# Optimization experiments

Measured on AMD Instinct MI355X. Metric: run time of the kernel, lower is better.

Reference implementation:

```python
import jax, jax.numpy as jnp
import numpy as np

H = 128  # hidden_size
I = 28   # input_size
C = 10   # num_classes


def setup_inputs() -> dict:
    key = jax.random.key(0)
    ks = jax.random.split(key, 11)
    s = 1.0 / np.sqrt(H)  # torch nn.RNN init scale
    return {
        "x": jax.random.normal(ks[0], (8192, 28, I), dtype=jnp.float32),
        "W_ih0": jax.random.uniform(ks[1], (H, I), jnp.float32, -s, s),
        "W_hh0": jax.random.uniform(ks[2], (H, H), jnp.float32, -s, s),
        "b_ih0": jax.random.uniform(ks[3], (H,), jnp.float32, -s, s),
        "b_hh0": jax.random.uniform(ks[4], (H,), jnp.float32, -s, s),
        "W_ih1": jax.random.uniform(ks[5], (H, H), jnp.float32, -s, s),
        "W_hh1": jax.random.uniform(ks[6], (H, H), jnp.float32, -s, s),
        "b_ih1": jax.random.uniform(ks[7], (H,), jnp.float32, -s, s),
        "b_hh1": jax.random.uniform(ks[8], (H,), jnp.float32, -s, s),
        "fc_w": jax.random.uniform(ks[9], (C, H), jnp.float32, -s, s),
        "fc_b": jax.random.uniform(ks[10], (C,), jnp.float32, -s, s),
    }


def _rnn_layer_full(x, W_ih, b_ih, W_hh, b_hh):
    # x: [B, T, D] -> full output sequence [B, T, H]
    B = x.shape[0]
    h0 = jnp.zeros((B, H), x.dtype)
    xw = jnp.einsum('btd,hd->bth', x, W_ih) + b_ih  # precompute input GEMM

    def step(h, xw_t):
        h = jnp.tanh(xw_t + h @ W_hh.T + b_hh)
        return h, h

    _, ys = jax.lax.scan(step, h0, jnp.swapaxes(xw, 0, 1))  # [T, B, H]
    return jnp.swapaxes(ys, 0, 1)


def _rnn_layer_last(x, W_ih, b_ih, W_hh, b_hh):
    # only the final hidden state is needed downstream
    B = x.shape[0]
    h0 = jnp.zeros((B, H), x.dtype)
    xw = jnp.einsum('btd,hd->bth', x, W_ih) + b_ih

    def step(h, xw_t):
        h = jnp.tanh(xw_t + h @ W_hh.T + b_hh)
        return h, None

    h_last, _ = jax.lax.scan(step, h0, jnp.swapaxes(xw, 0, 1))
    return h_last


def reference(x, W_ih0, W_hh0, b_ih0, b_hh0, W_ih1, W_hh1, b_ih1, b_hh1, fc_w, fc_b):
    out0 = _rnn_layer_full(x, W_ih0, b_ih0, W_hh0, b_hh0)   # [B, T, H]
    h_last = _rnn_layer_last(out0, W_ih1, b_ih1, W_hh1, b_hh1)  # [B, H] == out[:, -1, :]
    return h_last @ fc_w.T + fc_b  # [B, C]
```

## Files before the change

kernel.cpp:

```cpp
#include <hip/hip_runtime.h>

#define HSZ 128
#define ISZ 28
#define TSZ 28
#define CSZ 10
#define BT  16
#define NT  512
#define HP  136
#define XP  32

typedef _Float16 half_t;
typedef _Float16 v8h __attribute__((ext_vector_type(8)));
typedef _Float16 v4h __attribute__((ext_vector_type(4)));
typedef float v4f __attribute__((ext_vector_type(4)));

__device__ __forceinline__ float fast_tanh(float x) {
    float e = __expf(2.f * x);
    return 1.f - 2.f * __builtin_amdgcn_rcpf(e + 1.f);
}

__global__ __launch_bounds__(NT, 4)
void rnn_mfma4(const float* __restrict__ x,
               const float* __restrict__ W_ih0, const float* __restrict__ W_hh0,
               const float* __restrict__ b_ih0, const float* __restrict__ b_hh0,
               const float* __restrict__ W_ih1, const float* __restrict__ W_hh1,
               const float* __restrict__ b_ih1, const float* __restrict__ b_hh1,
               const float* __restrict__ fc_w, const float* __restrict__ fc_b,
               float* __restrict__ out)
{
    __shared__ half_t h0s[2][BT * HP];
    __shared__ half_t h1s[2][BT * HP];
    __shared__ half_t xs[TSZ][BT * XP];

    const int tid  = threadIdx.x;
    const int wave = tid >> 6;
    const int lane = tid & 63;
    const int ln   = lane & 15;
    const int quad = lane >> 4;
    const int kq   = quad * 8;
    const int b0   = blockIdx.x * BT;
    const int base = wave * 16;
    const int row  = base + ln;

    v8h aWx, aW0[4], aW1i[4], aW1h[4];
    v4f bias0, bias1;
    {
        float4 p = *(const float4*)(b_ih0 + base + quad * 4);
        float4 q = *(const float4*)(b_hh0 + base + quad * 4);
        bias0 = (v4f){p.x + q.x, p.y + q.y, p.z + q.z, p.w + q.w};
        p = *(const float4*)(b_ih1 + base + quad * 4);
        q = *(const float4*)(b_hh1 + base + quad * 4);
        bias1 = (v4f){p.x + q.x, p.y + q.y, p.z + q.z, p.w + q.w};
    }
    {
        const float* pw = W_ih0 + row * ISZ + kq;
        float4 a = *(const float4*)pw;
        float4 b = (kq < 24) ? *(const float4*)(pw + 4) : make_float4(0.f, 0.f, 0.f, 0.f);
        aWx = (v8h){(half_t)a.x, (half_t)a.y, (half_t)a.z, (half_t)a.w,
                    (half_t)b.x, (half_t)b.y, (half_t)b.z, (half_t)b.w};
    }
#pragma unroll
    for (int ks = 0; ks < 4; ++ks) {
        const float4* p0 = (const float4*)(W_hh0 + row * HSZ + ks * 32 + kq);
        const float4* p1 = (const float4*)(W_ih1 + row * HSZ + ks * 32 + kq);
        const float4* p2 = (const float4*)(W_hh1 + row * HSZ + ks * 32 + kq);
        float4 a = p0[0], b = p0[1];
        aW0[ks] = (v8h){(half_t)a.x, (half_t)a.y, (half_t)a.z, (half_t)a.w,
                        (half_t)b.x, (half_t)b.y, (half_t)b.z, (half_t)b.w};
        a = p1[0]; b = p1[1];
        aW1i[ks] = (v8h){(half_t)a.x, (half_t)a.y, (half_t)a.z, (half_t)a.w,
                         (half_t)b.x, (half_t)b.y, (half_t)b.z, (half_t)b.w};
        a = p2[0]; b = p2[1];
        aW1h[ks] = (v8h){(half_t)a.x, (half_t)a.y, (half_t)a.z, (half_t)a.w,
                         (half_t)b.x, (half_t)b.y, (half_t)b.z, (half_t)b.w};
    }

    {
        const float* xblk = x + (size_t)b0 * (TSZ * ISZ);
#pragma unroll
        for (int k = 0; k < 7; ++k) {
            const int F = tid + k * NT;
            if (F < BT * 196) {
                const int r   = F / 196;
                const int rem = F - r * 196;
                const int t   = rem / 7;
                const int i4  = (rem - t * 7) * 4;
                const float4 v = *(const float4*)(xblk + r * (TSZ * ISZ) + rem * 4);
                v4h p = {(half_t)v.x, (half_t)v.y, (half_t)v.z, (half_t)v.w};
                *(v4h*)&xs[t][r * XP + i4] = p;
            }
        }
        if (tid < TSZ * BT) {
            const int tt = tid >> 4, rr = tid & 15;
            *(v4h*)&xs[tt][rr * XP + ISZ] =
                (v4h){(half_t)0.f, (half_t)0.f, (half_t)0.f, (half_t)0.f};
        }
    }

    for (int idx = tid; idx < BT * HP; idx += NT)
        h1s[0][idx] = (half_t)0.f;
    __syncthreads();

    {
        const v8h bx = *(const v8h*)&xs[0][ln * XP + kq];
        v4f a0 = bias0;
        a0 = __builtin_amdgcn_mfma_f32_16x16x32_f16(aWx, bx, a0, 0, 0, 0);
        v4h p = {(half_t)fast_tanh(a0[0]), (half_t)fast_tanh(a0[1]),
                 (half_t)fast_tanh(a0[2]), (half_t)fast_tanh(a0[3])};
        *(v4h*)&h0s[0][ln * HP + base + quad * 4] = p;
    }
    __syncthreads();

#pragma unroll 2
    for (int t = 0; t < TSZ - 1; ++t) {
        const int pr = t & 1;

        v8h bh0[4], bh1[4];
#pragma unroll
        for (int ks = 0; ks < 4; ++ks) {
            bh0[ks] = *(const v8h*)&h0s[pr][ln * HP + ks * 32 + kq];
            bh1[ks] = *(const v8h*)&h1s[pr][ln * HP + ks * 32 + kq];
        }
        const v8h bx = *(const v8h*)&xs[t + 1][ln * XP + kq];

        v4f a0  = bias0;
        v4f a1i = bias1;
        v4f a1h = (v4f){0.f, 0.f, 0.f, 0.f};
        a0 = __builtin_amdgcn_mfma_f32_16x16x32_f16(aWx, bx, a0, 0, 0, 0);
#pragma unroll
        for (int ks = 0; ks < 4; ++ks) {
            a1i = __builtin_amdgcn_mfma_f32_16x16x32_f16(aW1i[ks], bh0[ks], a1i, 0, 0, 0);
            a1h = __builtin_amdgcn_mfma_f32_16x16x32_f16(aW1h[ks], bh1[ks], a1h, 0, 0, 0);
            a0  = __builtin_amdgcn_mfma_f32_16x16x32_f16(aW0[ks],  bh0[ks], a0,  0, 0, 0);
        }
        const v4f a1 = a1i + a1h;

        {
            v4h p1 = {(half_t)fast_tanh(a1[0]), (half_t)fast_tanh(a1[1]),
                      (half_t)fast_tanh(a1[2]), (half_t)fast_tanh(a1[3])};
            *(v4h*)&h1s[pr ^ 1][ln * HP + base + quad * 4] = p1;
            v4h p0 = {(half_t)fast_tanh(a0[0]), (half_t)fast_tanh(a0[1]),
                      (half_t)fast_tanh(a0[2]), (half_t)fast_tanh(a0[3])};
            *(v4h*)&h0s[pr ^ 1][ln * HP + base + quad * 4] = p0;
        }

        __syncthreads();
    }

    {
        const int pr = (TSZ - 1) & 1;
        v4f a1i = bias1;
        v4f a1h = (v4f){0.f, 0.f, 0.f, 0.f};
#pragma unroll
        for (int ks = 0; ks < 4; ++ks) {
            const v8h bh0 = *(const v8h*)&h0s[pr][ln * HP + ks * 32 + kq];
            const v8h bh1 = *(const v8h*)&h1s[pr][ln * HP + ks * 32 + kq];
            a1i = __builtin_amdgcn_mfma_f32_16x16x32_f16(aW1i[ks], bh0, a1i, 0, 0, 0);
            a1h = __builtin_amdgcn_mfma_f32_16x16x32_f16(aW1h[ks], bh1, a1h, 0, 0, 0);
        }
        const v4f a1 = a1i + a1h;
        v4h p1 = {(half_t)fast_tanh(a1[0]), (half_t)fast_tanh(a1[1]),
                  (half_t)fast_tanh(a1[2]), (half_t)fast_tanh(a1[3])};
        *(v4h*)&h1s[pr ^ 1][ln * HP + base + quad * 4] = p1;
    }
    __syncthreads();

    if (tid < BT * CSZ) {
        const int m = tid / CSZ, cc = tid - m * CSZ;
        float s = fc_b[cc];
#pragma unroll
        for (int k8 = 0; k8 < HSZ / 8; ++k8) {
            const v8h hv = *(const v8h*)&h1s[0][m * HP + k8 * 8];
            const float4 w0 = *(const float4*)(fc_w + cc * HSZ + k8 * 8);
            const float4 w1 = *(const float4*)(fc_w + cc * HSZ + k8 * 8 + 4);
            s += (float)hv[0] * w0.x + (float)hv[1] * w0.y +
                 (float)hv[2] * w0.z + (float)hv[3] * w0.w +
                 (float)hv[4] * w1.x + (float)hv[5] * w1.y +
                 (float)hv[6] * w1.z + (float)hv[7] * w1.w;
        }
        out[(b0 + m) * CSZ + cc] = s;
    }
}

extern "C" void kernel_launch(void* const* d_in, const int* in_sizes, int n_in,
                              void* d_out, int out_size, void* d_ws, size_t ws_size,
                              hipStream_t stream) {
    const float* x     = (const float*)d_in[0];
    const float* W_ih0 = (const float*)d_in[1];
    const float* W_hh0 = (const float*)d_in[2];
    const float* b_ih0 = (const float*)d_in[3];
    const float* b_hh0 = (const float*)d_in[4];
    const float* W_ih1 = (const float*)d_in[5];
    const float* W_hh1 = (const float*)d_in[6];
    const float* b_ih1 = (const float*)d_in[7];
    const float* b_hh1 = (const float*)d_in[8];
    const float* fc_w  = (const float*)d_in[9];
    const float* fc_b  = (const float*)d_in[10];
    float* out = (float*)d_out;

    const int B = in_sizes[0] / (TSZ * ISZ);
    dim3 grid(B / BT), block(NT);
    rnn_mfma4<<<grid, block, 0, stream>>>(x, W_ih0, W_hh0, b_ih0, b_hh0,
                                          W_ih1, W_hh1, b_ih1, b_hh1,
                                          fc_w, fc_b, out);
}
```

Baseline: 126.9 us.

## Process two 16-row batch groups per block and split MFMA accumulator chains

Doubles the batch tile per block to 32 rows, handled as two 16-row MFMA groups, so each wave reuses its register-resident weight fragments across twice as many sequences. Block count halves to 256, which leaves about one block per CU on a 256-CU part. The dependent MFMA accumulation chains are split into several independent partial accumulators so MFMAs from both groups can interleave and hide latency. The cost is higher register pressure (launch bounds lowered to 2 blocks/SM), more LDS, and fewer blocks to spread across the GPU.

New measurement: 128.9 us. About the same (+1.6%).

```diff
diff --git a/kernel.cpp b/kernel.cpp
--- a/kernel.cpp
+++ b/kernel.cpp
@@ -4,7 +4,8 @@
 #define ISZ 28
 #define TSZ 28
 #define CSZ 10
-#define BT  16
+#define BT  32
+#define NG  2
 #define NT  512
 #define HP  136
 #define XP  32
@@ -19,8 +20,8 @@
     return 1.f - 2.f * __builtin_amdgcn_rcpf(e + 1.f);
 }
 
-__global__ __launch_bounds__(NT, 4)
-void rnn_mfma4(const float* __restrict__ x,
+__global__ __launch_bounds__(NT, 2)
+void rnn_mfma5(const float* __restrict__ x,
                const float* __restrict__ W_ih0, const float* __restrict__ W_hh0,
                const float* __restrict__ b_ih0, const float* __restrict__ b_hh0,
                const float* __restrict__ W_ih1, const float* __restrict__ W_hh1,
@@ -78,7 +79,7 @@
     {
         const float* xblk = x + (size_t)b0 * (TSZ * ISZ);
 #pragma unroll
-        for (int k = 0; k < 7; ++k) {
+        for (int k = 0; k < 13; ++k) {
             const int F = tid + k * NT;
             if (F < BT * 196) {
                 const int r   = F / 196;
@@ -90,8 +91,8 @@
                 *(v4h*)&xs[t][r * XP + i4] = p;
             }
         }
-        if (tid < TSZ * BT) {
-            const int tt = tid >> 4, rr = tid & 15;
+        for (int idx = tid; idx < TSZ * BT; idx += NT) {
+            const int tt = idx >> 5, rr = idx & 31;
             *(v4h*)&xs[tt][rr * XP + ISZ] =
                 (v4h){(half_t)0.f, (half_t)0.f, (half_t)0.f, (half_t)0.f};
         }
@@ -101,13 +102,14 @@
         h1s[0][idx] = (half_t)0.f;
     __syncthreads();
 
-    {
-        const v8h bx = *(const v8h*)&xs[0][ln * XP + kq];
+#pragma unroll
+    for (int g = 0; g < NG; ++g) {
+        const v8h bx = *(const v8h*)&xs[0][(g * 16 + ln) * XP + kq];
         v4f a0 = bias0;
         a0 = __builtin_amdgcn_mfma_f32_16x16x32_f16(aWx, bx, a0, 0, 0, 0);
         v4h p = {(half_t)fast_tanh(a0[0]), (half_t)fast_tanh(a0[1]),
                  (half_t)fast_tanh(a0[2]), (half_t)fast_tanh(a0[3])};
-        *(v4h*)&h0s[0][ln * HP + base + quad * 4] = p;
+        *(v4h*)&h0s[0][(g * 16 + ln) * HP + base + quad * 4] = p;
     }
     __syncthreads();
 
@@ -115,33 +117,54 @@
     for (int t = 0; t < TSZ - 1; ++t) {
         const int pr = t & 1;
 
-        v8h bh0[4], bh1[4];
-#pragma unroll
-        for (int ks = 0; ks < 4; ++ks) {
-            bh0[ks] = *(const v8h*)&h0s[pr][ln * HP + ks * 32 + kq];
-            bh1[ks] = *(const v8h*)&h1s[pr][ln * HP + ks * 32 + kq];
-        }
-        const v8h bx = *(const v8h*)&xs[t + 1][ln * XP + kq];
-
-        v4f a0  = bias0;
-        v4f a1i = bias1;
-        v4f a1h = (v4f){0.f, 0.f, 0.f, 0.f};
-        a0 = __builtin_amdgcn_mfma_f32_16x16x32_f16(aWx, bx, a0, 0, 0, 0);
-#pragma unroll
-        for (int ks = 0; ks < 4; ++ks) {
-            a1i = __builtin_amdgcn_mfma_f32_16x16x32_f16(aW1i[ks], bh0[ks], a1i, 0, 0, 0);
-            a1h = __builtin_amdgcn_mfma_f32_16x16x32_f16(aW1h[ks], bh1[ks], a1h, 0, 0, 0);
-            a0  = __builtin_amdgcn_mfma_f32_16x16x32_f16(aW0[ks],  bh0[ks], a0,  0, 0, 0);
-        }
-        const v4f a1 = a1i + a1h;
-
-        {
+        v8h bh0[NG][4], bh1[NG][4], bx[NG];
+#pragma unroll
+        for (int g = 0; g < NG; ++g) {
+#pragma unroll
+            for (int ks = 0; ks < 4; ++ks)
+                bh0[g][ks] = *(const v8h*)&h0s[pr][(g * 16 + ln) * HP + ks * 32 + kq];
+            bx[g] = *(const v8h*)&xs[t + 1][(g * 16 + ln) * XP + kq];
+        }
+#pragma unroll
+        for (int g = 0; g < NG; ++g)
+#pragma unroll
+            for (int ks = 0; ks < 4; ++ks)
+                bh1[g][ks] = *(const v8h*)&h1s[pr][(g * 16 + ln) * HP + ks * 32 + kq];
+
+#pragma unroll
+        for (int g = 0; g < NG; ++g) {
+            v4f c0 = bias0;
+            c0 = __builtin_amdgcn_mfma_f32_16x16x32_f16(aWx, bx[g], c0, 0, 0, 0);
+            v4f c1 = (v4f){0.f, 0.f, 0.f, 0.f};
+            c1 = __builtin_amdgcn_mfma_f32_16x16x32_f16(aW0[0], bh0[g][0], c1, 0, 0, 0);
+            c1 = __builtin_amdgcn_mfma_f32_16x16x32_f16(aW0[1], bh0[g][1], c1, 0, 0, 0);
+            v4f c2 = (v4f){0.f, 0.f, 0.f, 0.f};
+            c2 = __builtin_amdgcn_mfma_f32_16x16x32_f16(aW0[2], bh0[g][2], c2, 0, 0, 0);
+            c2 = __builtin_amdgcn_mfma_f32_16x16x32_f16(aW0[3], bh0[g][3], c2, 0, 0, 0);
+            const v4f a0 = c0 + c1 + c2;
+            v4h p0 = {(half_t)fast_tanh(a0[0]), (half_t)fast_tanh(a0[1]),
+                      (half_t)fast_tanh(a0[2]), (half_t)fast_tanh(a0[3])};
+            *(v4h*)&h0s[pr ^ 1][(g * 16 + ln) * HP + base + quad * 4] = p0;
+        }
+
+#pragma unroll
+        for (int g = 0; g < NG; ++g) {
+            v4f s0 = bias1;
+            s0 = __builtin_amdgcn_mfma_f32_16x16x32_f16(aW1i[0], bh0[g][0], s0, 0, 0, 0);
+            s0 = __builtin_amdgcn_mfma_f32_16x16x32_f16(aW1i[1], bh0[g][1], s0, 0, 0, 0);
+            v4f s1 = (v4f){0.f, 0.f, 0.f, 0.f};
+            s1 = __builtin_amdgcn_mfma_f32_16x16x32_f16(aW1i[2], bh0[g][2], s1, 0, 0, 0);
+            s1 = __builtin_amdgcn_mfma_f32_16x16x32_f16(aW1i[3], bh0[g][3], s1, 0, 0, 0);
+            v4f s2 = (v4f){0.f, 0.f, 0.f, 0.f};
+            s2 = __builtin_amdgcn_mfma_f32_16x16x32_f16(aW1h[0], bh1[g][0], s2, 0, 0, 0);
+            s2 = __builtin_amdgcn_mfma_f32_16x16x32_f16(aW1h[1], bh1[g][1], s2, 0, 0, 0);
+            v4f s3 = (v4f){0.f, 0.f, 0.f, 0.f};
+            s3 = __builtin_amdgcn_mfma_f32_16x16x32_f16(aW1h[2], bh1[g][2], s3, 0, 0, 0);
+            s3 = __builtin_amdgcn_mfma_f32_16x16x32_f16(aW1h[3], bh1[g][3], s3, 0, 0, 0);
+            const v4f a1 = (s0 + s1) + (s2 + s3);
             v4h p1 = {(half_t)fast_tanh(a1[0]), (half_t)fast_tanh(a1[1]),
                       (half_t)fast_tanh(a1[2]), (half_t)fast_tanh(a1[3])};
-            *(v4h*)&h1s[pr ^ 1][ln * HP + base + quad * 4] = p1;
-            v4h p0 = {(half_t)fast_tanh(a0[0]), (half_t)fast_tanh(a0[1]),
-                      (half_t)fast_tanh(a0[2]), (half_t)fast_tanh(a0[3])};
-            *(v4h*)&h0s[pr ^ 1][ln * HP + base + quad * 4] = p0;
+            *(v4h*)&h1s[pr ^ 1][(g * 16 + ln) * HP + base + quad * 4] = p1;
         }
 
         __syncthreads();
@@ -149,19 +172,22 @@
 
     {
         const int pr = (TSZ - 1) & 1;
-        v4f a1i = bias1;
-        v4f a1h = (v4f){0.f, 0.f, 0.f, 0.f};
-#pragma unroll
-        for (int ks = 0; ks < 4; ++ks) {
-            const v8h bh0 = *(const v8h*)&h0s[pr][ln * HP + ks * 32 + kq];
-            const v8h bh1 = *(const v8h*)&h1s[pr][ln * HP + ks * 32 + kq];
-            a1i = __builtin_amdgcn_mfma_f32_16x16x32_f16(aW1i[ks], bh0, a1i, 0, 0, 0);
-            a1h = __builtin_amdgcn_mfma_f32_16x16x32_f16(aW1h[ks], bh1, a1h, 0, 0, 0);
-        }
-        const v4f a1 = a1i + a1h;
-        v4h p1 = {(half_t)fast_tanh(a1[0]), (half_t)fast_tanh(a1[1]),
-                  (half_t)fast_tanh(a1[2]), (half_t)fast_tanh(a1[3])};
-        *(v4h*)&h1s[pr ^ 1][ln * HP + base + quad * 4] = p1;
+#pragma unroll
+        for (int g = 0; g < NG; ++g) {
+            v4f s0 = bias1;
+            v4f s2 = (v4f){0.f, 0.f, 0.f, 0.f};
+#pragma unroll
+            for (int ks = 0; ks < 4; ++ks) {
+                const v8h bh0 = *(const v8h*)&h0s[pr][(g * 16 + ln) * HP + ks * 32 + kq];
+                const v8h bh1 = *(const v8h*)&h1s[pr][(g * 16 + ln) * HP + ks * 32 + kq];
+                s0 = __builtin_amdgcn_mfma_f32_16x16x32_f16(aW1i[ks], bh0, s0, 0, 0, 0);
+                s2 = __builtin_amdgcn_mfma_f32_16x16x32_f16(aW1h[ks], bh1, s2, 0, 0, 0);
+            }
+            const v4f a1 = s0 + s2;
+            v4h p1 = {(half_t)fast_tanh(a1[0]), (half_t)fast_tanh(a1[1]),
+                      (half_t)fast_tanh(a1[2]), (half_t)fast_tanh(a1[3])};
+            *(v4h*)&h1s[pr ^ 1][(g * 16 + ln) * HP + base + quad * 4] = p1;
+        }
     }
     __syncthreads();
 
@@ -200,7 +226,7 @@
 
     const int B = in_sizes[0] / (TSZ * ISZ);
     dim3 grid(B / BT), block(NT);
-    rnn_mfma4<<<grid, block, 0, stream>>>(x, W_ih0, W_hh0, b_ih0, b_hh0,
+    rnn_mfma5<<<grid, block, 0, stream>>>(x, W_ih0, W_hh0, b_ih0, b_hh0,
                                           W_ih1, W_hh1, b_ih1, b_hh1,
                                           fc_w, fc_b, out);
 }
```

## Halve waves per block, give each wave two row tiles, use fragment-ordered LDS layout

Applied to the files above, without the earlier changes.

Each block now runs 4 waves instead of 8, and each wave computes two 16-row output tiles. That halves the per-step shared-memory reads of the hidden-state B fragments per output and cuts the barrier participant count. Hidden states and inputs are stored in LDS in the exact MFMA B-fragment order (lane*8 contiguous), replacing padded row-major layouts to avoid bank conflicts and address math. In exchange it doubles the weight registers per thread and lowers the launch-bounds occupancy hint to 2, which could reduce latency hiding across blocks.

Measured after the change: 128.1 us. About the same (+1.0%).

```diff
diff --git a/kernel.cpp b/kernel.cpp
--- a/kernel.cpp
+++ b/kernel.cpp
@@ -5,9 +5,8 @@
 #define TSZ 28
 #define CSZ 10
 #define BT  16
-#define NT  512
-#define HP  136
-#define XP  32
+#define NT  256
+#define HBUF 2048
 
 typedef _Float16 half_t;
 typedef _Float16 v8h __attribute__((ext_vector_type(8)));
@@ -19,8 +18,8 @@
     return 1.f - 2.f * __builtin_amdgcn_rcpf(e + 1.f);
 }
 
-__global__ __launch_bounds__(NT, 4)
-void rnn_mfma4(const float* __restrict__ x,
+__global__ __launch_bounds__(NT, 2)
+void rnn_mfma6(const float* __restrict__ x,
                const float* __restrict__ W_ih0, const float* __restrict__ W_hh0,
                const float* __restrict__ b_ih0, const float* __restrict__ b_hh0,
                const float* __restrict__ W_ih1, const float* __restrict__ W_hh1,
@@ -28,86 +27,89 @@
                const float* __restrict__ fc_w, const float* __restrict__ fc_b,
                float* __restrict__ out)
 {
-    __shared__ half_t h0s[2][BT * HP];
-    __shared__ half_t h1s[2][BT * HP];
-    __shared__ half_t xs[TSZ][BT * XP];
+    __shared__ half_t h0s[2][HBUF];
+    __shared__ half_t h1s[2][HBUF];
+    __shared__ half_t xs[TSZ][512];
 
     const int tid  = threadIdx.x;
     const int wave = tid >> 6;
     const int lane = tid & 63;
     const int ln   = lane & 15;
     const int quad = lane >> 4;
-    const int kq   = quad * 8;
     const int b0   = blockIdx.x * BT;
-    const int base = wave * 16;
-    const int row  = base + ln;
-
-    v8h aWx, aW0[4], aW1i[4], aW1h[4];
-    v4f bias0, bias1;
+    const int wbase = wave * 32;
+
+    v8h aWx[2], aW0[2][4], aW1i[2][4], aW1h[2][4];
+    v4f bias0[2], bias1[2];
+#pragma unroll
+    for (int rt = 0; rt < 2; ++rt) {
+        const int row = wbase + rt * 16 + ln;
+        {
+            float4 p = *(const float4*)(b_ih0 + wbase + rt * 16 + quad * 4);
+            float4 q = *(const float4*)(b_hh0 + wbase + rt * 16 + quad * 4);
+            bias0[rt] = (v4f){p.x + q.x, p.y + q.y, p.z + q.z, p.w + q.w};
+            p = *(const float4*)(b_ih1 + wbase + rt * 16 + quad * 4);
+            q = *(const float4*)(b_hh1 + wbase + rt * 16 + quad * 4);
+            bias1[rt] = (v4f){p.x + q.x, p.y + q.y, p.z + q.z, p.w + q.w};
+        }
+        {
+            const float* pw = W_ih0 + row * ISZ + quad * 8;
+            float4 a = *(const float4*)pw;
+            float4 b = (quad < 3) ? *(const float4*)(pw + 4) : make_float4(0.f, 0.f, 0.f, 0.f);
+            aWx[rt] = (v8h){(half_t)a.x, (half_t)a.y, (half_t)a.z, (half_t)a.w,
+                            (half_t)b.x, (half_t)b.y, (half_t)b.z, (half_t)b.w};
+        }
+#pragma unroll
+        for (int ks = 0; ks < 4; ++ks) {
+            const float4* p0 = (const float4*)(W_hh0 + row * HSZ + ks * 32 + quad * 8);
+            const float4* p1 = (const float4*)(W_ih1 + row * HSZ + ks * 32 + quad * 8);
+            const float4* p2 = (const float4*)(W_hh1 + row * HSZ + ks * 32 + quad * 8);
+            float4 a = p0[0], b = p0[1];
+            aW0[rt][ks] = (v8h){(half_t)a.x, (half_t)a.y, (half_t)a.z, (half_t)a.w,
+                                (half_t)b.x, (half_t)b.y, (half_t)b.z, (half_t)b.w};
+            a = p1[0]; b = p1[1];
+            aW1i[rt][ks] = (v8h){(half_t)a.x, (half_t)a.y, (half_t)a.z, (half_t)a.w,
+                                 (half_t)b.x, (half_t)b.y, (half_t)b.z, (half_t)b.w};
+            a = p2[0]; b = p2[1];
+            aW1h[rt][ks] = (v8h){(half_t)a.x, (half_t)a.y, (half_t)a.z, (half_t)a.w,
+                                 (half_t)b.x, (half_t)b.y, (half_t)b.z, (half_t)b.w};
+        }
+    }
+
     {
-        float4 p = *(const float4*)(b_ih0 + base + quad * 4);
-        float4 q = *(const float4*)(b_hh0 + base + quad * 4);
-        bias0 = (v4f){p.x + q.x, p.y + q.y, p.z + q.z, p.w + q.w};
-        p = *(const float4*)(b_ih1 + base + quad * 4);
-        q = *(const float4*)(b_hh1 + base + quad * 4);
-        bias1 = (v4f){p.x + q.x, p.y + q.y, p.z + q.z, p.w + q.w};
-    }
+#pragma unroll
+        for (int it = 0; it < 7; ++it) {
+            const int c = tid + it * NT;
+            const int q = c & 3;
+            const int n = (c >> 2) & 15;
+            const int t = c >> 6;
+            const float* g = x + ((size_t)(b0 + n) * TSZ + t) * ISZ + q * 8;
+            float4 a = *(const float4*)g;
+            float4 b = (q < 3) ? *(const float4*)(g + 4) : make_float4(0.f, 0.f, 0.f, 0.f);
+            v8h p = {(half_t)a.x, (half_t)a.y, (half_t)a.z, (half_t)a.w,
+                     (half_t)b.x, (half_t)b.y, (half_t)b.z, (half_t)b.w};
+            *(v8h*)&xs[t][(q * 16 + n) * 8] = p;
+        }
+    }
+
+    *(v8h*)&h1s[0][tid * 8] = (v8h){(half_t)0.f, (half_t)0.f, (half_t)0.f, (half_t)0.f,
+                                    (half_t)0.f, (half_t)0.f, (half_t)0.f, (half_t)0.f};
+    __syncthreads();
+
+    const int ws0 = wave * 512 + (quad >> 1) * 128 + ln * 8 + (quad & 1) * 4;
+    const int ws1 = ws0 + 256;
+    const int ro = lane * 8;
+
     {
-        const float* pw = W_ih0 + row * ISZ + kq;
-        float4 a = *(const float4*)pw;
-        float4 b = (kq < 24) ? *(const float4*)(pw + 4) : make_float4(0.f, 0.f, 0.f, 0.f);
-        aWx = (v8h){(half_t)a.x, (half_t)a.y, (half_t)a.z, (half_t)a.w,
-                    (half_t)b.x, (half_t)b.y, (half_t)b.z, (half_t)b.w};
-    }
-#pragma unroll
-    for (int ks = 0; ks < 4; ++ks) {
-        const float4* p0 = (const float4*)(W_hh0 + row * HSZ + ks * 32 + kq);
-        const float4* p1 = (const float4*)(W_ih1 + row * HSZ + ks * 32 + kq);
-        const float4* p2 = (const float4*)(W_hh1 + row * HSZ + ks * 32 + kq);
-        float4 a = p0[0], b = p0[1];
-        aW0[ks] = (v8h){(half_t)a.x, (half_t)a.y, (half_t)a.z, (half_t)a.w,
-                        (half_t)b.x, (half_t)b.y, (half_t)b.z, (half_t)b.w};
-        a = p1[0]; b = p1[1];
-        aW1i[ks] = (v8h){(half_t)a.x, (half_t)a.y, (half_t)a.z, (half_t)a.w,
-                         (half_t)b.x, (half_t)b.y, (half_t)b.z, (half_t)b.w};
-        a = p2[0]; b = p2[1];
-        aW1h[ks] = (v8h){(half_t)a.x, (half_t)a.y, (half_t)a.z, (half_t)a.w,
-                         (half_t)b.x, (half_t)b.y, (half_t)b.z, (half_t)b.w};
-    }
-
-    {
-        const float* xblk = x + (size_t)b0 * (TSZ * ISZ);
-#pragma unroll
-        for (int k = 0; k < 7; ++k) {
-            const int F = tid + k * NT;
-            if (F < BT * 196) {
-                const int r   = F / 196;
-                const int rem = F - r * 196;
-                const int t   = rem / 7;
-                const int i4  = (rem - t * 7) * 4;
-                const float4 v = *(const float4*)(xblk + r * (TSZ * ISZ) + rem * 4);
-                v4h p = {(half_t)v.x, (half_t)v.y, (half_t)v.z, (half_t)v.w};
-                *(v4h*)&xs[t][r * XP + i4] = p;
-            }
-        }
-        if (tid < TSZ * BT) {
-            const int tt = tid >> 4, rr = tid & 15;
-            *(v4h*)&xs[tt][rr * XP + ISZ] =
-                (v4h){(half_t)0.f, (half_t)0.f, (half_t)0.f, (half_t)0.f};
-        }
-    }
-
-    for (int idx = tid; idx < BT * HP; idx += NT)
-        h1s[0][idx] = (half_t)0.f;
-    __syncthreads();
-
-    {
-        const v8h bx = *(const v8h*)&xs[0][ln * XP + kq];
-        v4f a0 = bias0;
-        a0 = __builtin_amdgcn_mfma_f32_16x16x32_f16(aWx, bx, a0, 0, 0, 0);
-        v4h p = {(half_t)fast_tanh(a0[0]), (half_t)fast_tanh(a0[1]),
-                 (half_t)fast_tanh(a0[2]), (half_t)fast_tanh(a0[3])};
-        *(v4h*)&h0s[0][ln * HP + base + quad * 4] = p;
+        const v8h bx = *(const v8h*)&xs[0][ro];
+#pragma unroll
+        for (int rt = 0; rt < 2; ++rt) {
+            v4f c = bias0[rt];
+            c = __builtin_amdgcn_mfma_f32_16x16x32_f16(aWx[rt], bx, c, 0, 0, 0);
+            v4h p = {(half_t)fast_tanh(c[0]), (half_t)fast_tanh(c[1]),
+                     (half_t)fast_tanh(c[2]), (half_t)fast_tanh(c[3])};
+            *(v4h*)&h0s[0][rt ? ws1 : ws0] = p;
+        }
     }
     __syncthreads();
 
@@ -117,31 +119,38 @@
 
         v8h bh0[4], bh1[4];
 #pragma unroll
-        for (int ks = 0; ks < 4; ++ks) {
-            bh0[ks] = *(const v8h*)&h0s[pr][ln * HP + ks * 32 + kq];
-            bh1[ks] = *(const v8h*)&h1s[pr][ln * HP + ks * 32 + kq];
-        }
-        const v8h bx = *(const v8h*)&xs[t + 1][ln * XP + kq];
-
-        v4f a0  = bias0;
-        v4f a1i = bias1;
-        v4f a1h = (v4f){0.f, 0.f, 0.f, 0.f};
-        a0 = __builtin_amdgcn_mfma_f32_16x16x32_f16(aWx, bx, a0, 0, 0, 0);
-#pragma unroll
-        for (int ks = 0; ks < 4; ++ks) {
-            a1i = __builtin_amdgcn_mfma_f32_16x16x32_f16(aW1i[ks], bh0[ks], a1i, 0, 0, 0);
-            a1h = __builtin_amdgcn_mfma_f32_16x16x32_f16(aW1h[ks], bh1[ks], a1h, 0, 0, 0);
-            a0  = __builtin_amdgcn_mfma_f32_16x16x32_f16(aW0[ks],  bh0[ks], a0,  0, 0, 0);
-        }
-        const v4f a1 = a1i + a1h;
-
-        {
-            v4h p1 = {(half_t)fast_tanh(a1[0]), (half_t)fast_tanh(a1[1]),
-                      (half_t)fast_tanh(a1[2]), (half_t)fast_tanh(a1[3])};
-            *(v4h*)&h1s[pr ^ 1][ln * HP + base + quad * 4] = p1;
-            v4h p0 = {(half_t)fast_tanh(a0[0]), (half_t)fast_tanh(a0[1]),
-                      (half_t)fast_tanh(a0[2]), (half_t)fast_tanh(a0[3])};
-            *(v4h*)&h0s[pr ^ 1][ln * HP + base + quad * 4] = p0;
+        for (int ks = 0; ks < 4; ++ks)
+            bh0[ks] = *(const v8h*)&h0s[pr][ks * 512 + ro];
+        const v8h bx = *(const v8h*)&xs[t + 1][ro];
+#pragma unroll
+        for (int ks = 0; ks < 4; ++ks)
+            bh1[ks] = *(const v8h*)&h1s[pr][ks * 512 + ro];
+
+#pragma unroll
+        for (int rt = 0; rt < 2; ++rt) {
+            v4f c = bias0[rt];
+            c = __builtin_amdgcn_mfma_f32_16x16x32_f16(aWx[rt], bx, c, 0, 0, 0);
+#pragma unroll
+            for (int ks = 0; ks < 4; ++ks)
+                c = __builtin_amdgcn_mfma_f32_16x16x32_f16(aW0[rt][ks], bh0[ks], c, 0, 0, 0);
+            v4h p = {(half_t)fast_tanh(c[0]), (half_t)fast_tanh(c[1]),
+                     (half_t)fast_tanh(c[2]), (half_t)fast_tanh(c[3])};
+            *(v4h*)&h0s[pr ^ 1][rt ? ws1 : ws0] = p;
+        }
+
+#pragma unroll
+        for (int rt = 0; rt < 2; ++rt) {
+            v4f si = bias1[rt];
+            v4f sh = (v4f){0.f, 0.f, 0.f, 0.f};
+#pragma unroll
+            for (int ks = 0; ks < 4; ++ks) {
+                si = __builtin_amdgcn_mfma_f32_16x16x32_f16(aW1i[rt][ks], bh0[ks], si, 0, 0, 0);
+                sh = __builtin_amdgcn_mfma_f32_16x16x32_f16(aW1h[rt][ks], bh1[ks], sh, 0, 0, 0);
+            }
+            const v4f a1 = si + sh;
+            v4h p = {(half_t)fast_tanh(a1[0]), (half_t)fast_tanh(a1[1]),
+                     (half_t)fast_tanh(a1[2]), (half_t)fast_tanh(a1[3])};
+            *(v4h*)&h1s[pr ^ 1][rt ? ws1 : ws0] = p;
         }
 
         __syncthreads();
@@ -149,19 +158,26 @@
 
     {
         const int pr = (TSZ - 1) & 1;
-        v4f a1i = bias1;
-        v4f a1h = (v4f){0.f, 0.f, 0.f, 0.f};
+        v8h bh0[4], bh1[4];
 #pragma unroll
         for (int ks = 0; ks < 4; ++ks) {
-            const v8h bh0 = *(const v8h*)&h0s[pr][ln * HP + ks * 32 + kq];
-            const v8h bh1 = *(const v8h*)&h1s[pr][ln * HP + ks * 32 + kq];
-            a1i = __builtin_amdgcn_mfma_f32_16x16x32_f16(aW1i[ks], bh0, a1i, 0, 0, 0);
-            a1h = __builtin_amdgcn_mfma_f32_16x16x32_f16(aW1h[ks], bh1, a1h, 0, 0, 0);
-        }
-        const v4f a1 = a1i + a1h;
-        v4h p1 = {(half_t)fast_tanh(a1[0]), (half_t)fast_tanh(a1[1]),
-                  (half_t)fast_tanh(a1[2]), (half_t)fast_tanh(a1[3])};
-        *(v4h*)&h1s[pr ^ 1][ln * HP + base + quad * 4] = p1;
+            bh0[ks] = *(const v8h*)&h0s[pr][ks * 512 + ro];
+            bh1[ks] = *(const v8h*)&h1s[pr][ks * 512 + ro];
+        }
+#pragma unroll
+        for (int rt = 0; rt < 2; ++rt) {
+            v4f si = bias1[rt];
+            v4f sh = (v4f){0.f, 0.f, 0.f, 0.f};
+#pragma unroll
+            for (int ks = 0; ks < 4; ++ks) {
+                si = __builtin_amdgcn_mfma_f32_16x16x32_f16(aW1i[rt][ks], bh0[ks], si, 0, 0, 0);
+                sh = __builtin_amdgcn_mfma_f32_16x16x32_f16(aW1h[rt][ks], bh1[ks], sh, 0, 0, 0);
+            }
+            const v4f a1 = si + sh;
+            v4h p = {(half_t)fast_tanh(a1[0]), (half_t)fast_tanh(a1[1]),
+                     (half_t)fast_tanh(a1[2]), (half_t)fast_tanh(a1[3])};
+            *(v4h*)&h1s[pr ^ 1][rt ? ws1 : ws0] = p;
+        }
     }
     __syncthreads();
 
@@ -169,14 +185,18 @@
         const int m = tid / CSZ, cc = tid - m * CSZ;
         float s = fc_b[cc];
 #pragma unroll
-        for (int k8 = 0; k8 < HSZ / 8; ++k8) {
-            const v8h hv = *(const v8h*)&h1s[0][m * HP + k8 * 8];
-            const float4 w0 = *(const float4*)(fc_w + cc * HSZ + k8 * 8);
-            const float4 w1 = *(const float4*)(fc_w + cc * HSZ + k8 * 8 + 4);
-            s += (float)hv[0] * w0.x + (float)hv[1] * w0.y +
-                 (float)hv[2] * w0.z + (float)hv[3] * w0.w +
-                 (float)hv[4] * w1.x + (float)hv[5] * w1.y +
-                 (float)hv[6] * w1.z + (float)hv[7] * w1.w;
+        for (int ks = 0; ks < 4; ++ks) {
+#pragma unroll
+            for (int q2 = 0; q2 < 4; ++q2) {
+                const v8h hv = *(const v8h*)&h1s[0][(ks * 64 + q2 * 16 + m) * 8];
+                const int kb = ks * 32 + q2 * 8;
+                const float4 w0 = *(const float4*)(fc_w + cc * HSZ + kb);
+                const float4 w1 = *(const float4*)(fc_w + cc * HSZ + kb + 4);
+                s += (float)hv[0] * w0.x + (float)hv[1] * w0.y +
+                     (float)hv[2] * w0.z + (float)hv[3] * w0.w +
+                     (float)hv[4] * w1.x + (float)hv[5] * w1.y +
+                     (float)hv[6] * w1.z + (float)hv[7] * w1.w;
+            }
         }
         out[(b0 + m) * CSZ + cc] = s;
     }
@@ -200,7 +220,7 @@
 
     const int B = in_sizes[0] / (TSZ * ISZ);
     dim3 grid(B / BT), block(NT);
-    rnn_mfma4<<<grid, block, 0, stream>>>(x, W_ih0, W_hh0, b_ih0, b_hh0,
+    rnn_mfma6<<<grid, block, 0, stream>>>(x, W_ih0, W_hh0, b_ih0, b_hh0,
                                           W_ih1, W_hh1, b_ih1, b_hh1,
                                           fc_w, fc_b, out);
 }
```
